# Kernel optimization log

Measured on AMD Instinct MI355X. Metric: run time of the kernel, lower is better.

Reference implementation:

```python
import jax, jax.numpy as jnp
import numpy as np

NHEADS = 16


def setup_inputs() -> dict:
    key = jax.random.key(0)
    ks = jax.random.split(key, 5)
    B, S, D = 2, 2048, 1024
    x = jax.random.normal(ks[0], (B, S, D), dtype=jnp.float32)
    W_packed = jax.random.normal(ks[1], (3 * D, D), dtype=jnp.float32) * (1.0 / np.sqrt(D))
    b_packed = jax.random.normal(ks[2], (3 * D,), dtype=jnp.float32) * 0.02
    W_out = jax.random.normal(ks[3], (D, D), dtype=jnp.float32) * (1.0 / np.sqrt(D))
    b_out = jax.random.normal(ks[4], (D,), dtype=jnp.float32) * 0.02
    return {"x": x, "W_packed": W_packed, "b_packed": b_packed, "W_out": W_out, "b_out": b_out}


def reference(x, W_packed, b_packed, W_out, b_out):
    B, S, D = x.shape
    H = NHEADS
    hd = D // H
    # packed QKV projection (self-attention: q is k is v)
    qkv = x @ W_packed.T + b_packed                       # [B,S,3D]
    q, k, v = jnp.split(qkv, 3, axis=-1)

    def heads(t):
        return t.reshape(B, S, H, hd).transpose(0, 2, 1, 3)  # [B,H,S,hd]

    q, k, v = map(heads, (q, k, v))

    # ALiBi slopes per flex path: exp2(-(h+1)*8/H)
    slopes = jnp.exp2(-(jnp.arange(1, H + 1, dtype=x.dtype) * (8.0 / H)))  # [H]
    pos = jnp.arange(S)
    rel = (pos[None, :] - pos[:, None]).astype(x.dtype)    # kv_idx - q_idx, [S,S]
    bias = slopes[:, None, None] * rel                     # [H,S,S]
    causal = pos[None, :] <= pos[:, None]                  # allowed positions
    neg = jnp.finfo(x.dtype).min
    attn_mask = jnp.where(causal[None, :, :], bias, neg)   # [H,S,S]

    scale = 1.0 / np.sqrt(hd)
    scores = jnp.einsum("bhqd,bhkd->bhqk", q, k) * scale + attn_mask[None]
    attn = jax.nn.softmax(scores, axis=-1)
    out = jnp.einsum("bhqk,bhkd->bhqd", attn, v)           # [B,H,S,hd]
    out = out.transpose(0, 2, 1, 3).reshape(B, S, D)
    return out @ W_out.T + b_out
```

## Files before the change

### kernel.cpp

```cpp
#include <hip/hip_runtime.h>

typedef float f32x4 __attribute__((ext_vector_type(4)));
typedef __bf16 bf16x8 __attribute__((ext_vector_type(8)));
typedef unsigned short u16;

__device__ __forceinline__ f32x4 mfma16(bf16x8 a, bf16x8 b, f32x4 c) {
  return __builtin_amdgcn_mfma_f32_16x16x32_bf16(a, b, c, 0, 0, 0);
}

__device__ __forceinline__ void gll16(const void* g, void* l) {
  __builtin_amdgcn_global_load_lds(
      (const __attribute__((address_space(1))) void*)g,
      (__attribute__((address_space(3))) void*)l, 16, 0, 0);
}

__global__ void cvt_kernel(const float* __restrict__ in, __bf16* __restrict__ out, int n8) {
  int idx = blockIdx.x * blockDim.x + threadIdx.x;
  int stride = gridDim.x * blockDim.x;
  for (int i = idx; i < n8; i += stride) {
    const float* p = in + (size_t)i * 8;
    f32x4 a = *(const f32x4*)p;
    f32x4 b = *(const f32x4*)(p + 4);
    bf16x8 r;
#pragma unroll
    for (int j = 0; j < 4; ++j) {
      r[j] = (__bf16)a[j];
      r[4 + j] = (__bf16)b[j];
    }
    *(bf16x8*)(out + (size_t)i * 8) = r;
  }
}

template <int BM, int BN, int MODE>
__global__ __launch_bounds__(256, 3) void gemm_bt(
    const u16* __restrict__ A, const u16* __restrict__ B,
    const float* __restrict__ bias, float* __restrict__ Cout,
    __bf16* __restrict__ qb, __bf16* __restrict__ kp, __bf16* __restrict__ vp,
    int M, int N, int K, int mtiles) {
  constexpr int MREP = BM / 32;
  constexpr int NREP = BN / 32;
  constexpr int LA = BM / 64;
  constexpr int LB = BN / 64;
  static_assert(LA + LB == 4, "vmcnt literals assume 4 loads/wave/step");
  __shared__ u16 lA[3 * BM * 32];
  __shared__ u16 lB[3 * BN * 32];
  const int tid = threadIdx.x;
  const int wid = tid >> 6;
  const int lane = tid & 63;
  const int lr = lane & 15;
  const int lg = lane >> 4;

  const int nwg = gridDim.x;
  const int lid = blockIdx.x;
  const int sw = (lid & 7) * (nwg >> 3) + (lid >> 3);
  const int bm = (sw % mtiles) * BM;
  const int bn = (sw / mtiles) * BN;

  const int wm = (wid >> 1) * (BM / 2);
  const int wn = (wid & 1) * (BN / 2);

  f32x4 acc[MREP][NREP] = {};

  auto stage = [&](int bf, int t) {
    const int kt = t * 32;
    char* baseA = (char*)lA + bf * (BM * 64);
    char* baseB = (char*)lB + bf * (BN * 64);
#pragma unroll
    for (int j = 0; j < LA; ++j) {
      int off = (tid + j * 256) * 16;
      gll16(A + (size_t)(bm + (off >> 6)) * K + kt + ((off & 63) >> 1),
            baseA + off);
    }
#pragma unroll
    for (int j = 0; j < LB; ++j) {
      int off = (tid + j * 256) * 16;
      gll16(B + (size_t)(bn + (off >> 6)) * K + kt + ((off & 63) >> 1),
            baseB + off);
    }
  };

  const int T = K / 32;
  stage(0, 0);
  stage(1, 1);
  stage(2, 2);

  for (int t = 0; t < T; ++t) {
    const int rem = T - 1 - t;
    if (rem >= 2)
      asm volatile("s_waitcnt vmcnt(8)" ::: "memory");
    else if (rem == 1)
      asm volatile("s_waitcnt vmcnt(4)" ::: "memory");
    else
      asm volatile("s_waitcnt vmcnt(0)" ::: "memory");
    __builtin_amdgcn_s_barrier();

    const u16* cA = lA + (t % 3) * BM * 32;
    const u16* cB = lB + (t % 3) * BN * 32;
    bf16x8 af[MREP], bfr[NREP];
#pragma unroll
    for (int mt = 0; mt < MREP; ++mt)
      af[mt] = *(const bf16x8*)&cA[(wm + mt * 16 + lr) * 32 + lg * 8];
#pragma unroll
    for (int nt = 0; nt < NREP; ++nt)
      bfr[nt] = *(const bf16x8*)&cB[(wn + nt * 16 + lr) * 32 + lg * 8];
#pragma unroll
    for (int mt = 0; mt < MREP; ++mt)
#pragma unroll
      for (int nt = 0; nt < NREP; ++nt)
        acc[mt][nt] = mfma16(af[mt], bfr[nt], acc[mt][nt]);

    __builtin_amdgcn_sched_barrier(0);
    __builtin_amdgcn_s_barrier();
    if (t + 3 < T) stage(t % 3, t + 3);
  }

#pragma unroll
  for (int nt = 0; nt < NREP; ++nt) {
    int col = bn + wn + nt * 16 + lr;
    float bv = bias[col];
#pragma unroll
    for (int mt = 0; mt < MREP; ++mt) {
#pragma unroll
      for (int r = 0; r < 4; ++r) {
        int row = bm + wm + mt * 16 + lg * 4 + r;
        float val = acc[mt][nt][r] + bv;
        if (MODE == 0) {
          Cout[(size_t)row * N + col] = val;
        } else {
          __bf16 bx = (__bf16)val;
          int b = row >> 11, s = row & 2047;
          int third = col >> 10, hd = col & 1023;
          int h = hd >> 6, d = hd & 63;
          if (third == 0) {
            qb[(size_t)row * 1024 + hd] = bx;
          } else {
            int bh = b * 16 + h, t2 = s >> 6, sr = s & 63;
            size_t tb = ((size_t)(bh * 32 + t2)) * 4096;
            if (third == 1)
              kp[tb + (sr >> 4) * 1024 + (d >> 5) * 512 + ((d >> 3) & 3) * 128 +
                 (sr & 15) * 8 + (d & 7)] = bx;
            else
              vp[tb + (d >> 4) * 1024 + (sr >> 5) * 512 + ((sr >> 3) & 3) * 128 +
                 (d & 15) * 8 + (sr & 7)] = bx;
          }
        }
      }
    }
  }
}

__global__ __launch_bounds__(64, 4) void attn_kernel(
    const __bf16* __restrict__ qb, const __bf16* __restrict__ kp,
    const __bf16* __restrict__ vp, __bf16* __restrict__ aout) {
  __shared__ __bf16 p_lds[16][72];
  const int lane = threadIdx.x & 63;
  const int lr = lane & 15;
  const int lg = lane >> 4;

  const int lid = blockIdx.x;
  const int xcd = lid & 7;
  const int rest = lid >> 3;
  const int bh = xcd * 4 + (rest & 3);
  const int a16 = 127 - (rest >> 2);
  const int b = bh >> 4, h = bh & 15;
  const int qr0 = a16 * 16;
  const int ntl = (a16 >> 2) + 1;

  const float LOG2E = 1.4426950408889634f;
  const float c1 = 0.125f * LOG2E;
  const float c2 = exp2f(-(float)(h + 1) * 0.5f) * LOG2E;

  bf16x8 ones;
#pragma unroll
  for (int j = 0; j < 8; ++j) ones[j] = (__bf16)1.0f;

  const u16* ktiles = (const u16*)kp + (size_t)bh * 32 * 4096;
  const u16* vtiles = (const u16*)vp + (size_t)bh * 32 * 4096;

  const __bf16* qrow = qb + (size_t)(b * 2048 + qr0 + lr) * 1024 + h * 64;
  bf16x8 qf0 = *(const bf16x8*)(qrow + lg * 8);
  bf16x8 qf1 = *(const bf16x8*)(qrow + 32 + lg * 8);

  float m[4], l[4], cq[4];
  f32x4 o[4];
#pragma unroll
  for (int r = 0; r < 4; ++r) {
    m[r] = 0.f;
    l[r] = 0.f;
    cq[r] = c2 * (float)(qr0 + lg * 4 + r);
  }
#pragma unroll
  for (int dt = 0; dt < 4; ++dt) o[dt] = (f32x4){0.f, 0.f, 0.f, 0.f};

  for (int t = 0; t < ntl; ++t) {
    const u16* kb = ktiles + (size_t)t * 4096;
    const u16* vb = vtiles + (size_t)t * 4096;
    const int kv = t * 64;
    const bool last = (t == ntl - 1);

    bf16x8 ka[8], va[8];
#pragma unroll
    for (int j = 0; j < 8; ++j)
      ka[j] = *(const bf16x8*)(kb + j * 512 + lane * 8);
#pragma unroll
    for (int j = 0; j < 8; ++j)
      va[j] = *(const bf16x8*)(vb + j * 512 + lane * 8);

    f32x4 s[4];
#pragma unroll
    for (int nt = 0; nt < 4; ++nt) {
      f32x4 tt = (f32x4){0.f, 0.f, 0.f, 0.f};
      tt = mfma16(qf0, ka[nt * 2], tt);
      tt = mfma16(qf1, ka[nt * 2 + 1], tt);
      s[nt] = tt;
    }

#pragma unroll
    for (int nt = 0; nt < 4; ++nt) {
      float bnt = c2 * (float)(kv + nt * 16 + lr);
#pragma unroll
      for (int r = 0; r < 4; ++r)
        s[nt][r] = __builtin_fmaf(s[nt][r], c1, bnt - cq[r]);
    }
    if (last) {
#pragma unroll
      for (int nt = 0; nt < 4; ++nt) {
        float kf = (float)(kv + nt * 16 + lr);
#pragma unroll
        for (int r = 0; r < 4; ++r) {
          float qi = (float)(qr0 + lg * 4 + r);
          if (kf > qi) s[nt][r] = -1e30f;
        }
      }
    }

    float pm[4];
#pragma unroll
    for (int r = 0; r < 4; ++r)
      pm[r] = fmaxf(fmaxf(s[0][r], s[1][r]), fmaxf(s[2][r], s[3][r]));
    bool ok = (pm[0] <= m[0] + 8.f) && (pm[1] <= m[1] + 8.f) &&
              (pm[2] <= m[2] + 8.f) && (pm[3] <= m[3] + 8.f);
    if (!__all(ok)) {
#pragma unroll
      for (int r = 0; r < 4; ++r)
#pragma unroll
        for (int d = 1; d < 16; d <<= 1)
          pm[r] = fmaxf(pm[r], __shfl_xor(pm[r], d));
#pragma unroll
      for (int r = 0; r < 4; ++r) {
        float mn = fmaxf(m[r], pm[r]);
        float fac = __builtin_amdgcn_exp2f(m[r] - mn);
        m[r] = mn;
        l[r] *= fac;
#pragma unroll
        for (int dt = 0; dt < 4; ++dt) o[dt][r] *= fac;
      }
    }

#pragma unroll
    for (int nt = 0; nt < 4; ++nt)
#pragma unroll
      for (int r = 0; r < 4; ++r) {
        float e = __builtin_amdgcn_exp2f(s[nt][r] - m[r]);
        p_lds[lg * 4 + r][nt * 16 + lr] = (__bf16)e;
      }

    bf16x8 pa0 = *(const bf16x8*)&p_lds[lr][lg * 8];
    bf16x8 pa1 = *(const bf16x8*)&p_lds[lr][32 + lg * 8];

    {
      f32x4 tt = (f32x4){0.f, 0.f, 0.f, 0.f};
      tt = mfma16(pa0, ones, tt);
      tt = mfma16(pa1, ones, tt);
#pragma unroll
      for (int r = 0; r < 4; ++r) l[r] += tt[r];
    }

#pragma unroll
    for (int dt = 0; dt < 4; ++dt) {
      o[dt] = mfma16(pa0, va[dt * 2], o[dt]);
      o[dt] = mfma16(pa1, va[dt * 2 + 1], o[dt]);
    }
  }

#pragma unroll
  for (int dt = 0; dt < 4; ++dt)
#pragma unroll
    for (int r = 0; r < 4; ++r) {
      float val = o[dt][r] / l[r];
      aout[(size_t)(b * 2048 + qr0 + lg * 4 + r) * 1024 + h * 64 + dt * 16 + lr] =
          (__bf16)val;
    }
}

extern "C" void kernel_launch(void* const* d_in, const int* in_sizes, int n_in,
                              void* d_out, int out_size, void* d_ws, size_t ws_size,
                              hipStream_t stream) {
  (void)in_sizes; (void)n_in; (void)out_size; (void)ws_size;
  const float* x = (const float*)d_in[0];
  const float* Wp = (const float*)d_in[1];
  const float* bp = (const float*)d_in[2];
  const float* Wo = (const float*)d_in[3];
  const float* bo = (const float*)d_in[4];
  float* out = (float*)d_out;

  char* ws = (char*)d_ws;
  u16* xb  = (u16*)(ws);
  u16* wpb = (u16*)(ws + (size_t)(8u << 20));
  u16* wob = (u16*)(ws + (size_t)(14u << 20));
  u16* qbp = (u16*)(ws + (size_t)(16u << 20));
  u16* kpp = (u16*)(ws + (size_t)(24u << 20));
  u16* vpp = (u16*)(ws + (size_t)(32u << 20));
  u16* ab  = xb;

  cvt_kernel<<<2048, 256, 0, stream>>>(x, (__bf16*)xb, 4096 * 1024 / 8);
  cvt_kernel<<<1536, 256, 0, stream>>>(Wp, (__bf16*)wpb, 3072 * 1024 / 8);
  cvt_kernel<<<512, 256, 0, stream>>>(Wo, (__bf16*)wob, 1024 * 1024 / 8);
  gemm_bt<128, 128, 1><<<768, 256, 0, stream>>>(
      xb, wpb, bp, nullptr, (__bf16*)qbp, (__bf16*)kpp, (__bf16*)vpp,
      4096, 3072, 1024, 32);
  attn_kernel<<<4096, 64, 0, stream>>>(
      (const __bf16*)qbp, (const __bf16*)kpp, (const __bf16*)vpp, (__bf16*)ab);
  gemm_bt<128, 128, 0><<<256, 256, 0, stream>>>(
      ab, wob, bo, out, nullptr, nullptr, nullptr, 4096, 1024, 1024, 32);
}
```

Before: 120.5 us.

## Fuse input conversions and use 256x256 eight-wave pipelined QKV GEMM

Merges the three fp32-to-bf16 conversion launches into one kernel that relies on the contiguous workspace layout (x, then Wp, then Wo). Replaces the 128x128 QKV projection GEMM with a 256x256 tile, 512-thread kernel using K=64 double-buffered LDS, XOR-swizzled LDS rows, and quarter-staged loads interleaved with four MFMA quadrants under s_setprio. The larger tile raises arithmetic intensity, and the interleaving aims to hide global loads behind compute. The cost is a grid of only 192 workgroups (under one wave of CUs on a 256-CU part), more barriers, and heavy register and LDS use.

```diff
diff --git a/kernel.cpp b/kernel.cpp
--- a/kernel.cpp
+++ b/kernel.cpp
@@ -14,13 +14,19 @@
       (__attribute__((address_space(3))) void*)l, 16, 0, 0);
 }
 
-__global__ void cvt_kernel(const float* __restrict__ in, __bf16* __restrict__ out, int n8) {
+__global__ void cvt3_kernel(const float* __restrict__ x,
+                            const float* __restrict__ wp,
+                            const float* __restrict__ wo,
+                            __bf16* __restrict__ out) {
   int idx = blockIdx.x * blockDim.x + threadIdx.x;
   int stride = gridDim.x * blockDim.x;
-  for (int i = idx; i < n8; i += stride) {
-    const float* p = in + (size_t)i * 8;
-    f32x4 a = *(const f32x4*)p;
-    f32x4 b = *(const f32x4*)(p + 4);
+  for (int i = idx; i < 1048576; i += stride) {
+    const float* src;
+    if (i < 524288) src = x + (size_t)i * 8;
+    else if (i < 917504) src = wp + (size_t)(i - 524288) * 8;
+    else src = wo + (size_t)(i - 917504) * 8;
+    f32x4 a = *(const f32x4*)src;
+    f32x4 b = *(const f32x4*)(src + 4);
     bf16x8 r;
 #pragma unroll
     for (int j = 0; j < 4; ++j) {
@@ -31,95 +37,150 @@
   }
 }
 
-template <int BM, int BN, int MODE>
-__global__ __launch_bounds__(256, 3) void gemm_bt(
+template <int MODE>
+__global__ __launch_bounds__(512, 2) void gemm8p(
     const u16* __restrict__ A, const u16* __restrict__ B,
     const float* __restrict__ bias, float* __restrict__ Cout,
     __bf16* __restrict__ qb, __bf16* __restrict__ kp, __bf16* __restrict__ vp,
     int M, int N, int K, int mtiles) {
-  constexpr int MREP = BM / 32;
-  constexpr int NREP = BN / 32;
-  constexpr int LA = BM / 64;
-  constexpr int LB = BN / 64;
-  static_assert(LA + LB == 4, "vmcnt literals assume 4 loads/wave/step");
-  __shared__ u16 lA[3 * BM * 32];
-  __shared__ u16 lB[3 * BN * 32];
+  __shared__ u16 lA[2 * 256 * 64];
+  __shared__ u16 lB[2 * 256 * 64];
   const int tid = threadIdx.x;
   const int wid = tid >> 6;
   const int lane = tid & 63;
-  const int lr = lane & 15;
-  const int lg = lane >> 4;
+  const int lr = lane & 15, lg = lane >> 4;
 
   const int nwg = gridDim.x;
   const int lid = blockIdx.x;
   const int sw = (lid & 7) * (nwg >> 3) + (lid >> 3);
-  const int bm = (sw % mtiles) * BM;
-  const int bn = (sw / mtiles) * BN;
-
-  const int wm = (wid >> 1) * (BM / 2);
-  const int wn = (wid & 1) * (BN / 2);
-
-  f32x4 acc[MREP][NREP] = {};
-
-  auto stage = [&](int bf, int t) {
-    const int kt = t * 32;
-    char* baseA = (char*)lA + bf * (BM * 64);
-    char* baseB = (char*)lB + bf * (BN * 64);
-#pragma unroll
-    for (int j = 0; j < LA; ++j) {
-      int off = (tid + j * 256) * 16;
-      gll16(A + (size_t)(bm + (off >> 6)) * K + kt + ((off & 63) >> 1),
-            baseA + off);
-    }
-#pragma unroll
-    for (int j = 0; j < LB; ++j) {
-      int off = (tid + j * 256) * 16;
-      gll16(B + (size_t)(bn + (off >> 6)) * K + kt + ((off & 63) >> 1),
-            baseB + off);
+  const int bm = (sw % mtiles) * 256;
+  const int bn = (sw / mtiles) * 256;
+  const int wm = (wid >> 2) * 128;
+  const int wn = (wid & 3) * 64;
+
+  f32x4 acc[8][4] = {};
+  const int KT = K >> 6;
+  const int NH = KT * 4;
+
+  auto stageh = [&](int h) {
+    const int kt = h >> 2, part = h & 3, slot = kt & 1;
+    const int kk = kt << 6;
+#pragma unroll
+    for (int j = 0; j < 2; ++j) {
+      int o16 = tid + j * 512;
+      int row = o16 >> 3;
+      int scb = ((o16 & 7) * 16) ^ ((row & 4) << 3);
+      if (part < 2)
+        gll16(A + (size_t)(bm + (part << 7) + row) * K + kk + (scb >> 1),
+              lA + slot * 16384 + (part << 13) + o16 * 8);
+      else
+        gll16(B + (size_t)(bn + ((part & 1) << 7) + row) * K + kk + (scb >> 1),
+              lB + slot * 16384 + ((part & 1) << 13) + o16 * 8);
     }
   };
 
-  const int T = K / 32;
-  stage(0, 0);
-  stage(1, 1);
-  stage(2, 2);
-
-  for (int t = 0; t < T; ++t) {
-    const int rem = T - 1 - t;
-    if (rem >= 2)
-      asm volatile("s_waitcnt vmcnt(8)" ::: "memory");
-    else if (rem == 1)
-      asm volatile("s_waitcnt vmcnt(4)" ::: "memory");
-    else
-      asm volatile("s_waitcnt vmcnt(0)" ::: "memory");
-    __builtin_amdgcn_s_barrier();
-
-    const u16* cA = lA + (t % 3) * BM * 32;
-    const u16* cB = lB + (t % 3) * BN * 32;
-    bf16x8 af[MREP], bfr[NREP];
-#pragma unroll
-    for (int mt = 0; mt < MREP; ++mt)
-      af[mt] = *(const bf16x8*)&cA[(wm + mt * 16 + lr) * 32 + lg * 8];
-#pragma unroll
-    for (int nt = 0; nt < NREP; ++nt)
-      bfr[nt] = *(const bf16x8*)&cB[(wn + nt * 16 + lr) * 32 + lg * 8];
-#pragma unroll
-    for (int mt = 0; mt < MREP; ++mt)
-#pragma unroll
-      for (int nt = 0; nt < NREP; ++nt)
-        acc[mt][nt] = mfma16(af[mt], bfr[nt], acc[mt][nt]);
-
-    __builtin_amdgcn_sched_barrier(0);
-    __builtin_amdgcn_s_barrier();
-    if (t + 3 < T) stage(t % 3, t + 3);
-  }
-
-#pragma unroll
-  for (int nt = 0; nt < NREP; ++nt) {
+  bf16x8 af[8][2], bfr[4][2];
+  auto rdA = [&](int slot, int mt, int ks) -> bf16x8 {
+    int row = wm + mt * 16 + lr;
+    int col = (ks * 32 + lg * 8) ^ ((row & 4) << 2);
+    return *(const bf16x8*)&lA[slot * 16384 + row * 64 + col];
+  };
+  auto rdB = [&](int slot, int nt, int ks) -> bf16x8 {
+    int row = wn + nt * 16 + lr;
+    int col = (ks * 32 + lg * 8) ^ ((row & 4) << 2);
+    return *(const bf16x8*)&lB[slot * 16384 + row * 64 + col];
+  };
+  auto quad = [&](int qm, int qn) {
+#pragma unroll
+    for (int mi = 0; mi < 4; ++mi)
+#pragma unroll
+      for (int ni = 0; ni < 2; ++ni)
+#pragma unroll
+        for (int ks = 0; ks < 2; ++ks) {
+          int mt = qm * 4 + mi, nt = qn * 2 + ni;
+          acc[mt][nt] = mfma16(af[mt][ks], bfr[nt][ks], acc[mt][nt]);
+        }
+  };
+
+#pragma unroll
+  for (int h = 0; h < 6; ++h) stageh(h);
+  __builtin_amdgcn_sched_barrier(0);
+  asm volatile("s_waitcnt vmcnt(4)" ::: "memory");
+  __builtin_amdgcn_s_barrier();
+
+  for (int kt = 0; kt < KT; ++kt) {
+    const int slot = kt & 1;
+    const int hb = kt * 4 + 6;
+#pragma unroll
+    for (int mt = 0; mt < 4; ++mt)
+#pragma unroll
+      for (int ks = 0; ks < 2; ++ks) af[mt][ks] = rdA(slot, mt, ks);
+#pragma unroll
+    for (int nt = 0; nt < 2; ++nt)
+#pragma unroll
+      for (int ks = 0; ks < 2; ++ks) bfr[nt][ks] = rdB(slot, nt, ks);
+    if (hb < NH) stageh(hb);
+    __builtin_amdgcn_sched_barrier(0);
+    __builtin_amdgcn_s_barrier();
+    asm volatile("s_waitcnt lgkmcnt(0)" ::: "memory");
+    __builtin_amdgcn_sched_barrier(0);
+    __builtin_amdgcn_s_setprio(1);
+    quad(0, 0);
+    __builtin_amdgcn_s_setprio(0);
+    __builtin_amdgcn_sched_barrier(0);
+    __builtin_amdgcn_s_barrier();
+#pragma unroll
+    for (int mt = 4; mt < 8; ++mt)
+#pragma unroll
+      for (int ks = 0; ks < 2; ++ks) af[mt][ks] = rdA(slot, mt, ks);
+#pragma unroll
+    for (int nt = 2; nt < 4; ++nt)
+#pragma unroll
+      for (int ks = 0; ks < 2; ++ks) bfr[nt][ks] = rdB(slot, nt, ks);
+    if (hb + 1 < NH) stageh(hb + 1);
+    __builtin_amdgcn_sched_barrier(0);
+    __builtin_amdgcn_s_barrier();
+    asm volatile("s_waitcnt lgkmcnt(0)" ::: "memory");
+    __builtin_amdgcn_sched_barrier(0);
+    __builtin_amdgcn_s_setprio(1);
+    quad(1, 0);
+    __builtin_amdgcn_s_setprio(0);
+    __builtin_amdgcn_sched_barrier(0);
+    __builtin_amdgcn_s_barrier();
+    if (hb + 2 < NH) stageh(hb + 2);
+    __builtin_amdgcn_sched_barrier(0);
+    __builtin_amdgcn_s_barrier();
+    __builtin_amdgcn_sched_barrier(0);
+    __builtin_amdgcn_s_setprio(1);
+    quad(0, 1);
+    __builtin_amdgcn_s_setprio(0);
+    __builtin_amdgcn_sched_barrier(0);
+    __builtin_amdgcn_s_barrier();
+    if (hb + 3 < NH) stageh(hb + 3);
+    __builtin_amdgcn_sched_barrier(0);
+    __builtin_amdgcn_s_barrier();
+    __builtin_amdgcn_sched_barrier(0);
+    __builtin_amdgcn_s_setprio(1);
+    quad(1, 1);
+    __builtin_amdgcn_s_setprio(0);
+    __builtin_amdgcn_sched_barrier(0);
+    if (kt + 1 < KT) {
+      if (4 * kt + 9 < NH)
+        asm volatile("s_waitcnt vmcnt(4)" ::: "memory");
+      else if (4 * kt + 8 < NH)
+        asm volatile("s_waitcnt vmcnt(2)" ::: "memory");
+      else
+        asm volatile("s_waitcnt vmcnt(0)" ::: "memory");
+    }
+    __builtin_amdgcn_s_barrier();
+  }
+
+#pragma unroll
+  for (int nt = 0; nt < 4; ++nt) {
     int col = bn + wn + nt * 16 + lr;
     float bv = bias[col];
 #pragma unroll
-    for (int mt = 0; mt < MREP; ++mt) {
+    for (int mt = 0; mt < 8; ++mt) {
 #pragma unroll
       for (int r = 0; r < 4; ++r) {
         int row = bm + wm + mt * 16 + lg * 4 + r;
@@ -149,6 +210,102 @@
   }
 }
 
+template <int BM, int BN, int MODE>
+__global__ __launch_bounds__(256, 3) void gemm_bt(
+    const u16* __restrict__ A, const u16* __restrict__ B,
+    const float* __restrict__ bias, float* __restrict__ Cout,
+    int M, int N, int K, int mtiles) {
+  constexpr int MREP = BM / 32;
+  constexpr int NREP = BN / 32;
+  constexpr int LA = BM / 64;
+  constexpr int LB = BN / 64;
+  static_assert(LA + LB == 4, "vmcnt literals assume 4 loads/wave/step");
+  __shared__ u16 lA[3 * BM * 32];
+  __shared__ u16 lB[3 * BN * 32];
+  const int tid = threadIdx.x;
+  const int wid = tid >> 6;
+  const int lane = tid & 63;
+  const int lr = lane & 15;
+  const int lg = lane >> 4;
+
+  const int nwg = gridDim.x;
+  const int lid = blockIdx.x;
+  const int sw = (lid & 7) * (nwg >> 3) + (lid >> 3);
+  const int bm = (sw % mtiles) * BM;
+  const int bn = (sw / mtiles) * BN;
+  const int wm = (wid >> 1) * (BM / 2);
+  const int wn = (wid & 1) * (BN / 2);
+
+  f32x4 acc[MREP][NREP] = {};
+
+  auto stage = [&](int bf, int t) {
+    const int kt = t * 32;
+    char* baseA = (char*)lA + bf * (BM * 64);
+    char* baseB = (char*)lB + bf * (BN * 64);
+#pragma unroll
+    for (int j = 0; j < LA; ++j) {
+      int off = (tid + j * 256) * 16;
+      gll16(A + (size_t)(bm + (off >> 6)) * K + kt + ((off & 63) >> 1),
+            baseA + off);
+    }
+#pragma unroll
+    for (int j = 0; j < LB; ++j) {
+      int off = (tid + j * 256) * 16;
+      gll16(B + (size_t)(bn + (off >> 6)) * K + kt + ((off & 63) >> 1),
+            baseB + off);
+    }
+  };
+
+  const int T = K / 32;
+  stage(0, 0);
+  stage(1, 1);
+  stage(2, 2);
+
+  for (int t = 0; t < T; ++t) {
+    const int rem = T - 1 - t;
+    if (rem >= 2)
+      asm volatile("s_waitcnt vmcnt(8)" ::: "memory");
+    else if (rem == 1)
+      asm volatile("s_waitcnt vmcnt(4)" ::: "memory");
+    else
+      asm volatile("s_waitcnt vmcnt(0)" ::: "memory");
+    __builtin_amdgcn_s_barrier();
+
+    const u16* cA = lA + (t % 3) * BM * 32;
+    const u16* cB = lB + (t % 3) * BN * 32;
+    bf16x8 af[MREP], bfr[NREP];
+#pragma unroll
+    for (int mt = 0; mt < MREP; ++mt)
+      af[mt] = *(const bf16x8*)&cA[(wm + mt * 16 + lr) * 32 + lg * 8];
+#pragma unroll
+    for (int nt = 0; nt < NREP; ++nt)
+      bfr[nt] = *(const bf16x8*)&cB[(wn + nt * 16 + lr) * 32 + lg * 8];
+#pragma unroll
+    for (int mt = 0; mt < MREP; ++mt)
+#pragma unroll
+      for (int nt = 0; nt < NREP; ++nt)
+        acc[mt][nt] = mfma16(af[mt], bfr[nt], acc[mt][nt]);
+
+    __builtin_amdgcn_sched_barrier(0);
+    __builtin_amdgcn_s_barrier();
+    if (t + 3 < T) stage(t % 3, t + 3);
+  }
+
+#pragma unroll
+  for (int nt = 0; nt < NREP; ++nt) {
+    int col = bn + wn + nt * 16 + lr;
+    float bv = bias[col];
+#pragma unroll
+    for (int mt = 0; mt < MREP; ++mt) {
+#pragma unroll
+      for (int r = 0; r < 4; ++r) {
+        int row = bm + wm + mt * 16 + lg * 4 + r;
+        Cout[(size_t)row * N + col] = acc[mt][nt][r] + bv;
+      }
+    }
+  }
+}
+
 __global__ __launch_bounds__(64, 4) void attn_kernel(
     const __bf16* __restrict__ qb, const __bf16* __restrict__ kp,
     const __bf16* __restrict__ vp, __bf16* __restrict__ aout) {
@@ -313,14 +470,12 @@
   u16* vpp = (u16*)(ws + (size_t)(32u << 20));
   u16* ab  = xb;
 
-  cvt_kernel<<<2048, 256, 0, stream>>>(x, (__bf16*)xb, 4096 * 1024 / 8);
-  cvt_kernel<<<1536, 256, 0, stream>>>(Wp, (__bf16*)wpb, 3072 * 1024 / 8);
-  cvt_kernel<<<512, 256, 0, stream>>>(Wo, (__bf16*)wob, 1024 * 1024 / 8);
-  gemm_bt<128, 128, 1><<<768, 256, 0, stream>>>(
+  cvt3_kernel<<<2048, 256, 0, stream>>>(x, Wp, Wo, (__bf16*)xb);
+  gemm8p<1><<<192, 512, 0, stream>>>(
       xb, wpb, bp, nullptr, (__bf16*)qbp, (__bf16*)kpp, (__bf16*)vpp,
-      4096, 3072, 1024, 32);
+      4096, 3072, 1024, 16);
   attn_kernel<<<4096, 64, 0, stream>>>(
       (const __bf16*)qbp, (const __bf16*)kpp, (const __bf16*)vpp, (__bf16*)ab);
   gemm_bt<128, 128, 0><<<256, 256, 0, stream>>>(
-      ab, wob, bo, out, nullptr, nullptr, nullptr, 4096, 1024, 1024, 32);
-}
+      ab, wob, bo, out, 4096, 1024, 1024, 32);
+}
```

After: 125.6 us. +4.2%, slower.
